# Kernel tuning notes

Measured on AMD Instinct MI355X. Metric: run time of the kernel, lower is better.

The kernel has to match this reference:

```python
import jax, jax.numpy as jnp
import numpy as np

EPS = 1e-6

def layernorm(x, alpha, bias):
    # torch.std default is unbiased (ddof=1)
    mean = x.mean(axis=-1, keepdims=True)
    std = jnp.std(x, axis=-1, keepdims=True, ddof=1)
    return alpha * (x - mean) / (std + EPS) + bias


def setup_inputs() -> dict:
    key = jax.random.key(0)
    B, L, d_model = 2, 1024, 1024
    d_state, d_conv, expand = 16, 4, 2
    d_inner = expand * d_model
    ks = jax.random.split(key, 8)
    std = 0.02
    x = jax.random.normal(ks[0], (B, L, d_model), dtype=jnp.float32)
    in_proj_w = jax.random.normal(ks[1], (2 * d_inner, d_model), dtype=jnp.float32) * std
    in_proj_b = jnp.zeros((2 * d_inner,), jnp.float32)
    conv_w = jax.random.normal(ks[2], (d_inner, 1, d_conv), dtype=jnp.float32) * std  # depthwise, groups=d_inner
    conv_b = jnp.zeros((d_inner,), jnp.float32)
    x_proj_w = jax.random.normal(ks[3], (2 * d_state, d_inner), dtype=jnp.float32) * std
    x_proj_b = jnp.zeros((2 * d_state,), jnp.float32)
    dt_proj_w = jax.random.normal(ks[4], (d_inner, d_inner), dtype=jnp.float32) * std
    dt_proj_b = jnp.zeros((d_inner,), jnp.float32)
    A_log = jnp.log(jnp.tile(jnp.arange(1, d_state + 1, dtype=jnp.float32), (d_inner, 1)))
    D = jnp.ones((d_inner,), jnp.float32)
    out_proj_w = jax.random.normal(ks[5], (d_model, d_inner), dtype=jnp.float32) * std
    out_proj_b = jnp.zeros((d_model,), jnp.float32)
    in_norm_alpha = jnp.ones((d_model,), jnp.float32)
    in_norm_bias = jnp.zeros((d_model,), jnp.float32)
    norm_alpha = jnp.ones((d_model,), jnp.float32)
    norm_bias = jnp.zeros((d_model,), jnp.float32)
    return {"x": x, "in_proj_w": in_proj_w, "in_proj_b": in_proj_b,
            "conv_w": conv_w, "conv_b": conv_b,
            "x_proj_w": x_proj_w, "x_proj_b": x_proj_b,
            "dt_proj_w": dt_proj_w, "dt_proj_b": dt_proj_b,
            "A_log": A_log, "D": D,
            "out_proj_w": out_proj_w, "out_proj_b": out_proj_b,
            "in_norm_alpha": in_norm_alpha, "in_norm_bias": in_norm_bias,
            "norm_alpha": norm_alpha, "norm_bias": norm_bias}


def reference(x, in_proj_w, in_proj_b, conv_w, conv_b, x_proj_w, x_proj_b,
              dt_proj_w, dt_proj_b, A_log, D, out_proj_w, out_proj_b,
              in_norm_alpha, in_norm_bias, norm_alpha, norm_bias):
    batch, L, d_model = x.shape
    d_inner = D.shape[0]
    d_state = A_log.shape[1]
    d_conv = conv_w.shape[-1]

    residual = x
    xn = layernorm(x, in_norm_alpha, in_norm_bias)
    xz = xn @ in_proj_w.T + in_proj_b                    # (B, L, 2*d_inner)
    x_in, z = jnp.split(xz, 2, axis=-1)

    # causal depthwise conv: torch pads both sides by d_conv-1 then slices [:L]
    # -> equivalent to left-pad only
    xc = jnp.swapaxes(x_in, 1, 2)                        # (B, d_inner, L)
    xc = jax.lax.conv_general_dilated(
        xc, conv_w, window_strides=(1,), padding=[(d_conv - 1, 0)],
        dimension_numbers=('NCH', 'OIH', 'NCH'),
        feature_group_count=d_inner) + conv_b[None, :, None]
    xc = jax.nn.silu(jnp.swapaxes(xc, 1, 2))             # (B, L, d_inner)

    Bmat, Cmat = jnp.split(xc @ x_proj_w.T + x_proj_b, 2, axis=-1)  # (B, L, d_state) each
    delta = jnp.clip(jax.nn.softplus(xc @ dt_proj_w.T + dt_proj_b), 1e-4, 10.0)
    A = -jnp.exp(A_log)                                  # (d_inner, d_state)
    flags = (jnp.arange(L) % 16) == 15                   # periodic renorm mask

    def step(h, inp):
        d_t, B_t, C_t, x_t, flag = inp                   # d_t,x_t: (B,d_inner); B_t,C_t: (B,d_state)
        dA = jnp.exp(jnp.clip(d_t[..., None] * A, -10.0, 0.0))      # (B,d_inner,d_state)
        dBx = d_t[..., None] * B_t[:, None, :] * x_t[..., None]
        h = dA * h + dBx
        hn = jnp.maximum(jnp.linalg.norm(h, axis=-1, keepdims=True), 1e-6)
        scale = jnp.where(hn > 10.0, 10.0 / hn, 1.0)
        h = jnp.where(flag, h * scale, h)
        y_t = jnp.sum(C_t[:, None, :] * h, axis=-1) + D * x_t
        return h, y_t

    h0 = jnp.zeros((batch, d_inner, d_state), dtype=x.dtype)
    xs = (jnp.swapaxes(delta, 0, 1), jnp.swapaxes(Bmat, 0, 1),
          jnp.swapaxes(Cmat, 0, 1), jnp.swapaxes(xc, 0, 1), flags)
    _, ys = jax.lax.scan(step, h0, xs)                   # ys: (L, B, d_inner)
    y = jnp.swapaxes(ys, 0, 1)

    y = y * jax.nn.silu(z)
    out = y @ out_proj_w.T + out_proj_b                  # dropout is identity in eval
    return layernorm(residual + out, norm_alpha, norm_bias)
```

## Files before the change

### kernel.cpp

```cpp
#include <hip/hip_runtime.h>
#include <math.h>

typedef unsigned short u16;
typedef unsigned int   u32;
typedef __bf16 bf16x8 __attribute__((ext_vector_type(8)));
typedef float  f32x4  __attribute__((ext_vector_type(4)));
typedef u16    u16x8  __attribute__((ext_vector_type(8)));

#define NB   2
#define LL   1024
#define DM   1024
#define DI   2048
#define MM   (NB*LL)
#define NXZ  (2*DI)
#define DSTATE 16
#define NSEG 64
#define NDT  2176
#define F32PAT 0x3F800000u

__device__ __forceinline__ float b2f(u16 u) {
  union { u32 i; float f; } v; v.i = ((u32)u) << 16; return v.f;
}
__device__ __forceinline__ u16 f2b(float f) {
  union { float f; u32 i; } v; v.f = f;
  u32 r = (v.i + 0x7FFFu + ((v.i >> 16) & 1u)) >> 16;
  return (u16)r;
}
__device__ __forceinline__ float ldx(const void* p, size_t i, bool isf32) {
  return isf32 ? ((const float*)p)[i] : b2f(((const u16*)p)[i]);
}

typedef __attribute__((address_space(1))) const void gas_t;
typedef __attribute__((address_space(3))) void las_t;
__device__ __forceinline__ void gload_lds16(const void* g, void* l) {
  __builtin_amdgcn_global_load_lds((gas_t*)g, (las_t*)l, 16, 0, 0);
}

__global__ __launch_bounds__(256) void ln1_kernel(
    const void* __restrict__ x, const void* __restrict__ alpha,
    const void* __restrict__ beta, u16* __restrict__ out,
    const u32* __restrict__ probe)
{
  const bool isf32 = (*probe == F32PAT);
  int row = blockIdx.x;
  int base = threadIdx.x * 4;
  size_t ix = (size_t)row * DM + base;
  float v0, v1, v2, v3;
  if (isf32) {
    float4 f = *(const float4*)((const float*)x + ix);
    v0 = f.x; v1 = f.y; v2 = f.z; v3 = f.w;
  } else {
    ushort4 u = *(const ushort4*)((const u16*)x + ix);
    v0 = b2f(u.x); v1 = b2f(u.y); v2 = b2f(u.z); v3 = b2f(u.w);
  }
  float s  = v0 + v1 + v2 + v3;
  float ss = v0*v0 + v1*v1 + v2*v2 + v3*v3;
#pragma unroll
  for (int off = 32; off > 0; off >>= 1) {
    s  += __shfl_down(s,  off);
    ss += __shfl_down(ss, off);
  }
  __shared__ float sb[4], ssb[4];
  int wv = threadIdx.x >> 6, ln = threadIdx.x & 63;
  if (ln == 0) { sb[wv] = s; ssb[wv] = ss; }
  __syncthreads();
  s  = sb[0]  + sb[1]  + sb[2]  + sb[3];
  ss = ssb[0] + ssb[1] + ssb[2] + ssb[3];
  float mean = s * (1.0f / DM);
  float var  = fmaxf((ss - (float)DM * mean * mean) * (1.0f / (DM - 1)), 0.0f);
  float inv  = 1.0f / (sqrtf(var) + 1e-6f);
  float a0 = ldx(alpha, base+0, isf32), a1 = ldx(alpha, base+1, isf32);
  float a2 = ldx(alpha, base+2, isf32), a3 = ldx(alpha, base+3, isf32);
  float b0 = ldx(beta,  base+0, isf32), b1 = ldx(beta,  base+1, isf32);
  float b2 = ldx(beta,  base+2, isf32), b3 = ldx(beta,  base+3, isf32);
  ushort4 o;
  o.x = f2b(a0 * (v0 - mean) * inv + b0);
  o.y = f2b(a1 * (v1 - mean) * inv + b1);
  o.z = f2b(a2 * (v2 - mean) * inv + b2);
  o.w = f2b(a3 * (v3 - mean) * inv + b3);
  *(ushort4*)(out + ix) = o;
}

__global__ __launch_bounds__(256) void ln2_kernel(
    const void* __restrict__ x, const float* __restrict__ outp,
    const void* __restrict__ alpha, const void* __restrict__ beta,
    void* __restrict__ out, const u32* __restrict__ probe)
{
  const bool isf32 = (*probe == F32PAT);
  int row = blockIdx.x;
  int base = threadIdx.x * 4;
  size_t ix = (size_t)row * DM + base;
  float v0, v1, v2, v3;
  if (isf32) {
    float4 f = *(const float4*)((const float*)x + ix);
    v0 = f.x; v1 = f.y; v2 = f.z; v3 = f.w;
  } else {
    ushort4 u = *(const ushort4*)((const u16*)x + ix);
    v0 = b2f(u.x); v1 = b2f(u.y); v2 = b2f(u.z); v3 = b2f(u.w);
  }
  float4 p = *(const float4*)(outp + ix);
  v0 += p.x; v1 += p.y; v2 += p.z; v3 += p.w;
  float s  = v0 + v1 + v2 + v3;
  float ss = v0*v0 + v1*v1 + v2*v2 + v3*v3;
#pragma unroll
  for (int off = 32; off > 0; off >>= 1) {
    s  += __shfl_down(s,  off);
    ss += __shfl_down(ss, off);
  }
  __shared__ float sb[4], ssb[4];
  int wv = threadIdx.x >> 6, ln = threadIdx.x & 63;
  if (ln == 0) { sb[wv] = s; ssb[wv] = ss; }
  __syncthreads();
  s  = sb[0]  + sb[1]  + sb[2]  + sb[3];
  ss = ssb[0] + ssb[1] + ssb[2] + ssb[3];
  float mean = s * (1.0f / DM);
  float var  = fmaxf((ss - (float)DM * mean * mean) * (1.0f / (DM - 1)), 0.0f);
  float inv  = 1.0f / (sqrtf(var) + 1e-6f);
  float a0 = ldx(alpha, base+0, isf32), a1 = ldx(alpha, base+1, isf32);
  float a2 = ldx(alpha, base+2, isf32), a3 = ldx(alpha, base+3, isf32);
  float b0 = ldx(beta,  base+0, isf32), b1 = ldx(beta,  base+1, isf32);
  float b2 = ldx(beta,  base+2, isf32), b3 = ldx(beta,  base+3, isf32);
  float r0 = a0 * (v0 - mean) * inv + b0;
  float r1 = a1 * (v1 - mean) * inv + b1;
  float r2 = a2 * (v2 - mean) * inv + b2;
  float r3 = a3 * (v3 - mean) * inv + b3;
  if (isf32) {
    float4 o; o.x = r0; o.y = r1; o.z = r2; o.w = r3;
    *(float4*)((float*)out + ix) = o;
  } else {
    ushort4 o; o.x = f2b(r0); o.y = f2b(r1); o.z = f2b(r2); o.w = f2b(r3);
    *(ushort4*)((u16*)out + ix) = o;
  }
}

__global__ __launch_bounds__(256) void ln2_sk_kernel(
    const void* __restrict__ x, const float* __restrict__ P,
    const void* __restrict__ op_bias,
    const void* __restrict__ alpha, const void* __restrict__ beta,
    void* __restrict__ out, const u32* __restrict__ probe)
{
  const bool isf32 = (*probe == F32PAT);
  int row = blockIdx.x;
  int base = threadIdx.x * 4;
  size_t ix = (size_t)row * DM + base;
  float v0, v1, v2, v3;
  if (isf32) {
    float4 f = *(const float4*)((const float*)x + ix);
    v0 = f.x; v1 = f.y; v2 = f.z; v3 = f.w;
  } else {
    ushort4 u = *(const ushort4*)((const u16*)x + ix);
    v0 = b2f(u.x); v1 = b2f(u.y); v2 = b2f(u.z); v3 = b2f(u.w);
  }
  v0 += ldx(op_bias, base+0, isf32);
  v1 += ldx(op_bias, base+1, isf32);
  v2 += ldx(op_bias, base+2, isf32);
  v3 += ldx(op_bias, base+3, isf32);
#pragma unroll
  for (int sk = 0; sk < 4; ++sk) {
    float4 p = *(const float4*)(P + ((size_t)sk * MM + row) * DM + base);
    v0 += p.x; v1 += p.y; v2 += p.z; v3 += p.w;
  }
  float s  = v0 + v1 + v2 + v3;
  float ss = v0*v0 + v1*v1 + v2*v2 + v3*v3;
#pragma unroll
  for (int off = 32; off > 0; off >>= 1) {
    s  += __shfl_down(s,  off);
    ss += __shfl_down(ss, off);
  }
  __shared__ float sb[4], ssb[4];
  int wv = threadIdx.x >> 6, ln = threadIdx.x & 63;
  if (ln == 0) { sb[wv] = s; ssb[wv] = ss; }
  __syncthreads();
  s  = sb[0]  + sb[1]  + sb[2]  + sb[3];
  ss = ssb[0] + ssb[1] + ssb[2] + ssb[3];
  float mean = s * (1.0f / DM);
  float var  = fmaxf((ss - (float)DM * mean * mean) * (1.0f / (DM - 1)), 0.0f);
  float inv  = 1.0f / (sqrtf(var) + 1e-6f);
  float a0 = ldx(alpha, base+0, isf32), a1 = ldx(alpha, base+1, isf32);
  float a2 = ldx(alpha, base+2, isf32), a3 = ldx(alpha, base+3, isf32);
  float b0 = ldx(beta,  base+0, isf32), b1 = ldx(beta,  base+1, isf32);
  float b2 = ldx(beta,  base+2, isf32), b3 = ldx(beta,  base+3, isf32);
  float r0 = a0 * (v0 - mean) * inv + b0;
  float r1 = a1 * (v1 - mean) * inv + b1;
  float r2 = a2 * (v2 - mean) * inv + b2;
  float r3 = a3 * (v3 - mean) * inv + b3;
  if (isf32) {
    float4 o; o.x = r0; o.y = r1; o.z = r2; o.w = r3;
    *(float4*)((float*)out + ix) = o;
  } else {
    ushort4 o; o.x = f2b(r0); o.y = f2b(r1); o.z = f2b(r2); o.w = f2b(r3);
    *(ushort4*)((u16*)out + ix) = o;
  }
}

#define CVT_A  4194304u
#define CVT_B  8388608u
#define CVT_C 10485760u
#define CVT_D 10551296u
#define CVT_E 10747904u

__global__ __launch_bounds__(256) void cvt_kernel(
    const void* __restrict__ s_in, const void* __restrict__ s_dt,
    const void* __restrict__ s_op, const void* __restrict__ s_xp,
    u16* __restrict__ inpw, u16* __restrict__ wdt, u16* __restrict__ opw,
    const u32* __restrict__ probe)
{
  const bool isf32 = (*probe == F32PAT);
  size_t i4 = ((size_t)blockIdx.x * 256 + threadIdx.x) * 4;
  if (i4 >= CVT_E) return;
  const void* src; u16* dst; size_t off;
  if      (i4 < CVT_A) { src = s_in; dst = inpw;        off = i4; }
  else if (i4 < CVT_B) { src = s_dt; dst = wdt;         off = i4 - CVT_A; }
  else if (i4 < CVT_C) { src = s_op; dst = opw;         off = i4 - CVT_B; }
  else if (i4 < CVT_D) { src = s_xp; dst = wdt + CVT_A; off = i4 - CVT_C; }
  else {
    ushort4 z = {0, 0, 0, 0};
    *(ushort4*)(wdt + 4259840u + (i4 - CVT_D)) = z;
    return;
  }
  ushort4 o;
  if (isf32) {
    float4 f = *(const float4*)((const float*)src + off);
    o.x = f2b(f.x); o.y = f2b(f.y); o.z = f2b(f.z); o.w = f2b(f.w);
  } else {
    o = *(const ushort4*)((const u16*)src + off);
  }
  *(ushort4*)(dst + off) = o;
}

#define EPI_NONE 0
#define EPI_SOFTPLUS 1

template<int EPI, int OUTBF>
__global__ __launch_bounds__(256) void gemm_fast(
    const u16* __restrict__ A, const u16* __restrict__ W,
    const void* __restrict__ bias, void* __restrict__ Cout,
    const u32* __restrict__ probe, int M, int N, int K)
{
  __shared__ __align__(16) u16 As[128 * 32];
  __shared__ __align__(16) u16 Ws[128 * 32];
  const bool isf32 = (*probe == F32PAT);
  const int tid  = threadIdx.x;
  const int wave = tid >> 6;
  const int lane = tid & 63;
  const int quad = lane >> 4;
  const int l16  = lane & 15;
  const int m0 = blockIdx.x * 128;
  const int n0 = blockIdx.y * 128;
  const int wm = (wave >> 1) * 64;
  const int wn = (wave & 1) * 64;

  f32x4 acc[4][4] = {};

  for (int k0 = 0; k0 < K; k0 += 32) {
    __syncthreads();
#pragma unroll
    for (int q = 0; q < 2; ++q) {
      int ci  = wave * 128 + q * 64 + lane;
      int row = ci >> 2;
      int kc  = (ci & 3) * 8;
      const u16* ga = A + (size_t)(m0 + row) * K + k0 + kc;
      const u16* gw = W + (size_t)(n0 + row) * K + k0 + kc;
      u16* la = As + (size_t)(wave * 128 + q * 64) * 8;
      u16* lw = Ws + (size_t)(wave * 128 + q * 64) * 8;
      gload_lds16(ga, la);
      gload_lds16(gw, lw);
    }
    __syncthreads();
    bf16x8 af[4], bfr[4];
#pragma unroll
    for (int i = 0; i < 4; ++i) {
      af[i]  = *(const bf16x8*)(As + (size_t)(wm + i * 16 + l16) * 32 + quad * 8);
      bfr[i] = *(const bf16x8*)(Ws + (size_t)(wn + i * 16 + l16) * 32 + quad * 8);
    }
#pragma unroll
    for (int i = 0; i < 4; ++i)
#pragma unroll
      for (int j = 0; j < 4; ++j)
        acc[i][j] = __builtin_amdgcn_mfma_f32_16x16x32_bf16(af[i], bfr[j], acc[i][j], 0, 0, 0);
  }

#pragma unroll
  for (int i = 0; i < 4; ++i) {
    int rbase = m0 + wm + i * 16 + quad * 4;
#pragma unroll
    for (int j = 0; j < 4; ++j) {
      int col = n0 + wn + j * 16 + l16;
      float bv = ldx(bias, col, isf32);
#pragma unroll
      for (int r = 0; r < 4; ++r) {
        float v = acc[i][j][r] + bv;
        if (EPI == EPI_SOFTPLUS) {
          v = (v > 20.0f) ? v : __logf(1.0f + __expf(v));
          v = fminf(fmaxf(v, 1e-4f), 10.0f);
        }
        size_t oi = (size_t)(rbase + r) * N + col;
        if (OUTBF) ((u16*)Cout)[oi] = f2b(v);
        else       ((float*)Cout)[oi] = v;
      }
    }
  }
}

__global__ __launch_bounds__(256) void gemm_sk(
    const u16* __restrict__ A, const u16* __restrict__ W,
    float* __restrict__ P, int M, int N, int Kfull, int Kslice)
{
  __shared__ __align__(16) u16 As[128 * 32];
  __shared__ __align__(16) u16 Ws[128 * 32];
  const int tid  = threadIdx.x;
  const int wave = tid >> 6;
  const int lane = tid & 63;
  const int quad = lane >> 4;
  const int l16  = lane & 15;
  const int m0 = blockIdx.x * 128;
  const int n0 = blockIdx.y * 128;
  const int sk = blockIdx.z;
  const int kbeg = sk * Kslice;
  const int kend = kbeg + Kslice;
  const int wm = (wave >> 1) * 64;
  const int wn = (wave & 1) * 64;

  f32x4 acc[4][4] = {};

  for (int k0 = kbeg; k0 < kend; k0 += 32) {
    __syncthreads();
#pragma unroll
    for (int q = 0; q < 2; ++q) {
      int ci  = wave * 128 + q * 64 + lane;
      int row = ci >> 2;
      int kc  = (ci & 3) * 8;
      const u16* ga = A + (size_t)(m0 + row) * Kfull + k0 + kc;
      const u16* gw = W + (size_t)(n0 + row) * Kfull + k0 + kc;
      u16* la = As + (size_t)(wave * 128 + q * 64) * 8;
      u16* lw = Ws + (size_t)(wave * 128 + q * 64) * 8;
      gload_lds16(ga, la);
      gload_lds16(gw, lw);
    }
    __syncthreads();
    bf16x8 af[4], bfr[4];
#pragma unroll
    for (int i = 0; i < 4; ++i) {
      af[i]  = *(const bf16x8*)(As + (size_t)(wm + i * 16 + l16) * 32 + quad * 8);
      bfr[i] = *(const bf16x8*)(Ws + (size_t)(wn + i * 16 + l16) * 32 + quad * 8);
    }
#pragma unroll
    for (int i = 0; i < 4; ++i)
#pragma unroll
      for (int j = 0; j < 4; ++j)
        acc[i][j] = __builtin_amdgcn_mfma_f32_16x16x32_bf16(af[i], bfr[j], acc[i][j], 0, 0, 0);
  }

  float* Pb = P + (size_t)sk * M * N;
#pragma unroll
  for (int i = 0; i < 4; ++i) {
    int rbase = m0 + wm + i * 16 + quad * 4;
#pragma unroll
    for (int j = 0; j < 4; ++j) {
      int col = n0 + wn + j * 16 + l16;
#pragma unroll
      for (int r = 0; r < 4; ++r)
        Pb[(size_t)(rbase + r) * N + col] = acc[i][j][r];
    }
  }
}

__global__ __launch_bounds__(256) void reduce_combo(
    const float* __restrict__ P, const void* __restrict__ bias_dt,
    const void* __restrict__ bias_xp, float* __restrict__ delta,
    float* __restrict__ bc, const u32* __restrict__ probe)
{
  const bool isf32 = (*probe == F32PAT);
  const int m = blockIdx.x;
  const float* p0 = P + (size_t)m * NDT;
  const float* p1 = P + (size_t)(MM + m) * NDT;
  for (int n = threadIdx.x; n < DI + 32; n += 256) {
    float v = p0[n] + p1[n];
    if (n < DI) {
      v += ldx(bias_dt, n, isf32);
      v = (v > 20.0f) ? v : __logf(1.0f + __expf(v));
      v = fminf(fmaxf(v, 1e-4f), 10.0f);
      delta[(size_t)m * DI + n] = v;
    } else {
      bc[(size_t)m * 32 + (n - DI)] = v + ldx(bias_xp, n - DI, isf32);
    }
  }
}

template<int EPI, int OUTBF>
__global__ __launch_bounds__(256) void gemm_r2(
    const u16* __restrict__ A, const void* __restrict__ W,
    const void* __restrict__ bias, void* __restrict__ Cout,
    const u32* __restrict__ probe, int M, int N, int K)
{
  __shared__ __align__(16) u16 As[128 * 32];
  __shared__ __align__(16) u16 Ws[128 * 32];
  const bool isf32 = (*probe == F32PAT);
  const int tid  = threadIdx.x;
  const int wave = tid >> 6;
  const int lane = tid & 63;
  const int quad = lane >> 4;
  const int l16  = lane & 15;
  const int m0 = blockIdx.x * 128;
  const int n0 = blockIdx.y * 128;
  const int wm = (wave >> 1) * 64;
  const int wn = (wave & 1) * 64;

  f32x4 acc[4][4] = {};

  for (int k0 = 0; k0 < K; k0 += 32) {
    u16x8 va[2], vw[2];
#pragma unroll
    for (int q = 0; q < 2; ++q) {
      int ci  = wave * 128 + q * 64 + lane;
      int row = ci >> 2;
      int kc  = (ci & 3) * 8;
      va[q] = *(const u16x8*)(A + (size_t)(m0 + row) * K + k0 + kc);
      size_t wi = (size_t)(n0 + row) * K + k0 + kc;
      if (isf32) {
        const float* Wf = (const float*)W;
        float4 f0 = *(const float4*)(Wf + wi);
        float4 f1 = *(const float4*)(Wf + wi + 4);
        u16x8 t;
        t[0] = f2b(f0.x); t[1] = f2b(f0.y); t[2] = f2b(f0.z); t[3] = f2b(f0.w);
        t[4] = f2b(f1.x); t[5] = f2b(f1.y); t[6] = f2b(f1.z); t[7] = f2b(f1.w);
        vw[q] = t;
      } else {
        vw[q] = *(const u16x8*)((const u16*)W + wi);
      }
    }
    __syncthreads();
#pragma unroll
    for (int q = 0; q < 2; ++q) {
      int ci = wave * 128 + q * 64 + lane;
      *(u16x8*)(As + (size_t)ci * 8) = va[q];
      *(u16x8*)(Ws + (size_t)ci * 8) = vw[q];
    }
    __syncthreads();
    bf16x8 af[4], bfr[4];
#pragma unroll
    for (int i = 0; i < 4; ++i) {
      af[i]  = *(const bf16x8*)(As + (size_t)(wm + i * 16 + l16) * 32 + quad * 8);
      bfr[i] = *(const bf16x8*)(Ws + (size_t)(wn + i * 16 + l16) * 32 + quad * 8);
    }
#pragma unroll
    for (int i = 0; i < 4; ++i)
#pragma unroll
      for (int j = 0; j < 4; ++j)
        acc[i][j] = __builtin_amdgcn_mfma_f32_16x16x32_bf16(af[i], bfr[j], acc[i][j], 0, 0, 0);
  }

#pragma unroll
  for (int i = 0; i < 4; ++i) {
    int rbase = m0 + wm + i * 16 + quad * 4;
#pragma unroll
    for (int j = 0; j < 4; ++j) {
      int col = n0 + wn + j * 16 + l16;
      float bv = ldx(bias, col, isf32);
#pragma unroll
      for (int r = 0; r < 4; ++r) {
        float v = acc[i][j][r] + bv;
        if (EPI == EPI_SOFTPLUS) {
          v = (v > 20.0f) ? v : __logf(1.0f + __expf(v));
          v = fminf(fmaxf(v, 1e-4f), 10.0f);
        }
        size_t oi = (size_t)(rbase + r) * N + col;
        if (OUTBF) ((u16*)Cout)[oi] = f2b(v);
        else       ((float*)Cout)[oi] = v;
      }
    }
  }
}

__global__ __launch_bounds__(256) void conv_silu_kernel(
    const u16* __restrict__ xz, const void* __restrict__ cw,
    const void* __restrict__ cb, u16* __restrict__ xc_bf,
    const u32* __restrict__ probe)
{
  const bool isf32 = (*probe == F32PAT);
  int g = blockIdx.x * 256 + threadIdx.x;
  int c = g & (DI - 1);
  int m = g >> 11;
  int l = m & (LL - 1);
  float w0 = ldx(cw, c*4+0, isf32), w1 = ldx(cw, c*4+1, isf32);
  float w2 = ldx(cw, c*4+2, isf32), w3 = ldx(cw, c*4+3, isf32);
  const u16* col = xz + (size_t)m * NXZ + c;
  float acc = ldx(cb, c, isf32);
  acc += w3 * b2f(col[0]);
  if (l >= 1) acc += w2 * b2f(*(col - NXZ));
  if (l >= 2) acc += w1 * b2f(*(col - 2*NXZ));
  if (l >= 3) acc += w0 * b2f(*(col - 3*NXZ));
  float sil = acc / (1.0f + __expf(-acc));
  xc_bf[g] = f2b(sil);
}

__global__ __launch_bounds__(256) void proj_bc_r2(
    const u16* __restrict__ xc, const void* __restrict__ W,
    const void* __restrict__ bias, float* __restrict__ bc,
    const u32* __restrict__ probe)
{
  const bool isf32 = (*probe == F32PAT);
  int m = blockIdx.x;
  int n = threadIdx.x >> 3;
  int part = threadIdx.x & 7;
  const u16* xr = xc + (size_t)m * DI + part * 256;
  size_t wbase = (size_t)n * DI + part * 256;
  float acc = 0.0f;
  if (isf32) {
    const float* wr = (const float*)W + wbase;
#pragma unroll 8
    for (int i = 0; i < 256; i += 4) {
      ushort4 xv = *(const ushort4*)(xr + i);
      float4  wv = *(const float4*)(wr + i);
      acc += b2f(xv.x)*wv.x + b2f(xv.y)*wv.y + b2f(xv.z)*wv.z + b2f(xv.w)*wv.w;
    }
  } else {
    const u16* wr = (const u16*)W + wbase;
#pragma unroll 8
    for (int i = 0; i < 256; i += 4) {
      ushort4 xv = *(const ushort4*)(xr + i);
      ushort4 wv = *(const ushort4*)(wr + i);
      acc += b2f(xv.x)*b2f(wv.x) + b2f(xv.y)*b2f(wv.y)
           + b2f(xv.z)*b2f(wv.z) + b2f(xv.w)*b2f(wv.w);
    }
  }
  __shared__ float ps[256];
  ps[threadIdx.x] = acc;
  __syncthreads();
  if (threadIdx.x < 32) {
    float s = 0.0f;
#pragma unroll
    for (int p = 0; p < 8; ++p) s += ps[threadIdx.x * 8 + p];
    bc[(size_t)m * 32 + threadIdx.x] = s + ldx(bias, threadIdx.x, isf32);
  }
}

__global__ __launch_bounds__(256, 4) void scan_p1(
    const float* __restrict__ delta, const float* __restrict__ bc,
    const u16* __restrict__ xc, const void* __restrict__ A_log,
    float2* __restrict__ PQ, const u32* __restrict__ probe)
{
  const bool isf32 = (*probe == F32PAT);
  const int c = blockIdx.x * 256 + threadIdx.x;
  const int g = blockIdx.y;
  const int b = blockIdx.z;
  const int row0 = b * LL + g * 16;
  __shared__ float sBC[512];
  if (threadIdx.x < 128)
    *(float4*)&sBC[threadIdx.x * 4] =
        *(const float4*)(bc + (size_t)row0 * 32 + threadIdx.x * 4);
  float Av2[16];
#pragma unroll
  for (int s = 0; s < 16; ++s)
    Av2[s] = -__expf(ldx(A_log, (size_t)c * DSTATE + s, isf32)) * 1.44269504f;
  float p[16], q[16];
#pragma unroll
  for (int s = 0; s < 16; ++s) { p[s] = 1.0f; q[s] = 0.0f; }
  __syncthreads();
  const float CLIP2 = -14.4269504f;
#pragma unroll 4
  for (int j = 0; j < 16; ++j) {
    int row = row0 + j;
    float d  = delta[(size_t)row * DI + c];
    float x  = b2f(xc[(size_t)row * DI + c]);
    float dx = d * x;
    float4 B4[4];
    B4[0] = *(const float4*)&sBC[j * 32 + 0];
    B4[1] = *(const float4*)&sBC[j * 32 + 4];
    B4[2] = *(const float4*)&sBC[j * 32 + 8];
    B4[3] = *(const float4*)&sBC[j * 32 + 12];
    const float* Bv = (const float*)B4;
#pragma unroll
    for (int s = 0; s < 16; ++s) {
      float a = __builtin_amdgcn_exp2f(fmaxf(d * Av2[s], CLIP2));
      q[s] = a * q[s] + dx * Bv[s];
      p[s] *= a;
    }
  }
  float2* out = PQ + ((size_t)(b * NSEG + g) * DI + c) * DSTATE;
#pragma unroll
  for (int s = 0; s < 16; ++s) out[s] = make_float2(p[s], q[s]);
}

__global__ __launch_bounds__(256) void scan_p2(
    const float2* __restrict__ PQ, float* __restrict__ Hin,
    float* __restrict__ Scale)
{
  const int s = threadIdx.x & 15;
  const int c = blockIdx.x * 16 + (threadIdx.x >> 4);
  const int b = blockIdx.y;
  const size_t stride = (size_t)DI * DSTATE;
  const size_t base = ((size_t)b * NSEG * DI + c) * DSTATE + s;
  float h = 0.0f;
  float2 pq = PQ[base];
  for (int g = 0; g < NSEG; ++g) {
    float2 cur = pq;
    if (g < NSEG - 1) pq = PQ[base + (size_t)(g + 1) * stride];
    Hin[base + (size_t)g * stride] = h;
    h = cur.x * h + cur.y;
    float n2 = h * h;
    n2 += __shfl_xor(n2, 1);
    n2 += __shfl_xor(n2, 2);
    n2 += __shfl_xor(n2, 4);
    n2 += __shfl_xor(n2, 8);
    float hn = fmaxf(sqrtf(n2), 1e-6f);
    float sc = hn > 10.0f ? 10.0f / hn : 1.0f;
    if (s == 0) Scale[((size_t)b * NSEG + g) * DI + c] = sc;
    h *= sc;
  }
}

__global__ __launch_bounds__(256, 4) void scan_p3(
    const float* __restrict__ delta, const float* __restrict__ bc,
    const u16* __restrict__ xc, const u16* __restrict__ xz,
    const void* __restrict__ A_log, const void* __restrict__ Dp,
    const float* __restrict__ Hin, const float* __restrict__ Scale,
    u16* __restrict__ y_bf, const u32* __restrict__ probe)
{
  const bool isf32 = (*probe == F32PAT);
  const int c = blockIdx.x * 256 + threadIdx.x;
  const int g = blockIdx.y;
  const int b = blockIdx.z;
  const int row0 = b * LL + g * 16;
  __shared__ float sBC[512];
  if (threadIdx.x < 128)
    *(float4*)&sBC[threadIdx.x * 4] =
        *(const float4*)(bc + (size_t)row0 * 32 + threadIdx.x * 4);
  float Av2[16];
#pragma unroll
  for (int s = 0; s < 16; ++s)
    Av2[s] = -__expf(ldx(A_log, (size_t)c * DSTATE + s, isf32)) * 1.44269504f;
  float h[16];
  const float* hp = Hin + ((size_t)(b * NSEG + g) * DI + c) * DSTATE;
#pragma unroll
  for (int s4 = 0; s4 < 4; ++s4)
    *(float4*)&h[s4 * 4] = *(const float4*)(hp + s4 * 4);
  const float sc15 = Scale[((size_t)b * NSEG + g) * DI + c];
  const float Dc = ldx(Dp, c, isf32);
  __syncthreads();
  const float CLIP2 = -14.4269504f;
#pragma unroll 4
  for (int j = 0; j < 16; ++j) {
    int row = row0 + j;
    float d  = delta[(size_t)row * DI + c];
    float x  = b2f(xc[(size_t)row * DI + c]);
    float z  = b2f(xz[(size_t)row * NXZ + DI + c]);
    float dx = d * x;
    float4 BC[8];
    BC[0] = *(const float4*)&sBC[j * 32 + 0];
    BC[1] = *(const float4*)&sBC[j * 32 + 4];
    BC[2] = *(const float4*)&sBC[j * 32 + 8];
    BC[3] = *(const float4*)&sBC[j * 32 + 12];
    BC[4] = *(const float4*)&sBC[j * 32 + 16];
    BC[5] = *(const float4*)&sBC[j * 32 + 20];
    BC[6] = *(const float4*)&sBC[j * 32 + 24];
    BC[7] = *(const float4*)&sBC[j * 32 + 28];
    const float* Bv = (const float*)BC;
    const float* Cv = Bv + 16;
#pragma unroll
    for (int s = 0; s < 16; ++s) {
      float a = __builtin_amdgcn_exp2f(fmaxf(d * Av2[s], CLIP2));
      h[s] = a * h[s] + dx * Bv[s];
    }
    if (j == 15) {
#pragma unroll
      for (int s = 0; s < 16; ++s) h[s] *= sc15;
    }
    float ys = 0.0f;
#pragma unroll
    for (int s = 0; s < 16; ++s) ys += Cv[s] * h[s];
    float yo = (ys + Dc * x) * (z / (1.0f + __expf(-z)));
    y_bf[(size_t)row * DI + c] = f2b(yo);
  }
}

__global__ __launch_bounds__(256) void scan_mono(
    const float* __restrict__ delta, const float* __restrict__ bc,
    const u16* __restrict__ xc, const u16* __restrict__ xz,
    const void* __restrict__ A_log, const void* __restrict__ Dp,
    u16* __restrict__ y_bf, const u32* __restrict__ probe)
{
  const bool isf32 = (*probe == F32PAT);
  const int s = threadIdx.x & 15;
  const int c = blockIdx.x * 16 + (threadIdx.x >> 4);
  const int b = blockIdx.y;
  const float Av2 = -__expf(ldx(A_log, (size_t)c * DSTATE + s, isf32)) * 1.44269504f;
  const float Dc  = ldx(Dp, c, isf32);
  const float CLIP2 = -14.4269504f;
  float h = 0.0f;
  for (int t0 = 0; t0 < LL; t0 += 16) {
    float dl[16], xl[16], zl[16], Bv[16], Cv[16];
#pragma unroll
    for (int j = 0; j < 16; ++j) {
      int row = b * LL + t0 + j;
      dl[j] = delta[(size_t)row * DI + c];
      xl[j] = b2f(xc[(size_t)row * DI + c]);
      zl[j] = b2f(xz[(size_t)row * NXZ + DI + c]);
      Bv[j] = bc[(size_t)row * 32 + s];
      Cv[j] = bc[(size_t)row * 32 + 16 + s];
    }
#pragma unroll
    for (int j = 0; j < 16; ++j) {
      float d = dl[j], x = xl[j];
      float dA = __builtin_amdgcn_exp2f(fmaxf(d * Av2, CLIP2));
      h = dA * h + (d * x) * Bv[j];
      if (j == 15) {
        float n2 = h * h;
        n2 += __shfl_xor(n2, 1); n2 += __shfl_xor(n2, 2);
        n2 += __shfl_xor(n2, 4); n2 += __shfl_xor(n2, 8);
        float hn = fmaxf(sqrtf(n2), 1e-6f);
        float sc = hn > 10.0f ? 10.0f / hn : 1.0f;
        h *= sc;
      }
      float ys = Cv[j] * h;
      ys += __shfl_xor(ys, 1); ys += __shfl_xor(ys, 2);
      ys += __shfl_xor(ys, 4); ys += __shfl_xor(ys, 8);
      float z = zl[j];
      float yo = (ys + Dc * x) * (z / (1.0f + __expf(-z)));
      if (s == 0) {
        int row = b * LL + t0 + j;
        y_bf[(size_t)row * DI + c] = f2b(yo);
      }
    }
  }
}

extern "C" void kernel_launch(void* const* d_in, const int* in_sizes, int n_in,
                              void* d_out, int out_size, void* d_ws, size_t ws_size,
                              hipStream_t stream) {
  const void* x          = d_in[0];
  const void* in_proj_w  = d_in[1];
  const void* in_proj_b  = d_in[2];
  const void* conv_w     = d_in[3];
  const void* conv_b     = d_in[4];
  const void* x_proj_w   = d_in[5];
  const void* x_proj_b   = d_in[6];
  const void* dt_proj_w  = d_in[7];
  const void* dt_proj_b  = d_in[8];
  const void* A_log      = d_in[9];
  const void* Dp         = d_in[10];
  const void* out_proj_w = d_in[11];
  const void* out_proj_b = d_in[12];
  const void* in_norm_a  = d_in[13];
  const void* in_norm_b  = d_in[14];
  const void* norm_a     = d_in[15];
  const void* norm_b     = d_in[16];
  const u32*  probe      = (const u32*)d_in[13];

  const size_t MiB = 1048576;
  const size_t NEED_NEW = 106299392;

  if (ws_size >= NEED_NEW) {
    char* w = (char*)d_ws;
    u16*   xz_bf = (u16*)w;    w += 16 * MiB;
    u16*   xc_bf = (u16*)w;    w += 8 * MiB;
    float* delta = (float*)w;  w += 16 * MiB;
    float* bc    = (float*)w;  w += 256 * 1024;
    float* Scale = (float*)w;  w += 1 * MiB;
    u16*   opw   = (u16*)w;    w += 4 * MiB;
    u16*   y_bf  = (u16*)w;    w += 8 * MiB;
    char* S = w;
    u16*    wdt    = (u16*)(S);
    u16*    inpw   = (u16*)(S + 8*MiB + 512*1024);
    u16*    xn_bf  = (u16*)(S + 16*MiB + 512*1024);
    float*  deltaP = (float*)(S + 8*MiB + 512*1024);
    float2* PQ     = (float2*)(S);
    float*  Hin    = (float*)(S + 32*MiB);
    float*  outP   = (float*)(S);

    cvt_kernel<<<10496, 256, 0, stream>>>(in_proj_w, dt_proj_w, out_proj_w, x_proj_w,
                                          inpw, wdt, opw, probe);
    ln1_kernel<<<MM, 256, 0, stream>>>(x, in_norm_a, in_norm_b, xn_bf, probe);
    gemm_fast<EPI_NONE, 1><<<dim3(MM/128, NXZ/128), 256, 0, stream>>>(
        xn_bf, inpw, in_proj_b, xz_bf, probe, MM, NXZ, DM);
    conv_silu_kernel<<<(MM * DI) / 256, 256, 0, stream>>>(xz_bf, conv_w, conv_b, xc_bf, probe);
    gemm_sk<<<dim3(MM/128, NDT/128, 2), 256, 0, stream>>>(
        xc_bf, wdt, deltaP, MM, NDT, DI, DI/2);
    reduce_combo<<<MM, 256, 0, stream>>>(deltaP, dt_proj_b, x_proj_b, delta, bc, probe);
    scan_p1<<<dim3(DI/256, NSEG, NB), 256, 0, stream>>>(delta, bc, xc_bf, A_log, PQ, probe);
    scan_p2<<<dim3(DI/16, NB), 256, 0, stream>>>(PQ, Hin, Scale);
    scan_p3<<<dim3(DI/256, NSEG, NB), 256, 0, stream>>>(
        delta, bc, xc_bf, xz_bf, A_log, Dp, Hin, Scale, y_bf, probe);
    gemm_sk<<<dim3(MM/128, DM/128, 4), 256, 0, stream>>>(
        y_bf, opw, outP, MM, DM, DI, DI/4);
    ln2_sk_kernel<<<MM, 256, 0, stream>>>(x, outP, out_proj_b, norm_a, norm_b, d_out, probe);
  } else {
    char* w = (char*)d_ws;
    u16*   xn_bf = (u16*)w;   w += (size_t)MM * DM * 2;
    u16*   xz_bf = (u16*)w;   w += (size_t)MM * NXZ * 2;
    u16*   xc_bf = (u16*)w;   w += (size_t)MM * DI * 2;
    float* delta = (float*)w; w += (size_t)MM * DI * 4;
    float* bc    = (float*)w; w += (size_t)MM * 32 * 4;
    u16*   y_bf  = (u16*)w;   w += (size_t)MM * DI * 2;
    float* outp  = (float*)w; w += (size_t)MM * DM * 4;

    ln1_kernel<<<MM, 256, 0, stream>>>(x, in_norm_a, in_norm_b, xn_bf, probe);
    gemm_r2<EPI_NONE, 1><<<dim3(MM/128, NXZ/128), 256, 0, stream>>>(
        xn_bf, in_proj_w, in_proj_b, xz_bf, probe, MM, NXZ, DM);
    conv_silu_kernel<<<(MM * DI) / 256, 256, 0, stream>>>(xz_bf, conv_w, conv_b, xc_bf, probe);
    gemm_r2<EPI_SOFTPLUS, 0><<<dim3(MM/128, DI/128), 256, 0, stream>>>(
        xc_bf, dt_proj_w, dt_proj_b, delta, probe, MM, DI, DI);
    proj_bc_r2<<<MM, 256, 0, stream>>>(xc_bf, x_proj_w, x_proj_b, bc, probe);
    scan_mono<<<dim3(DI/16, NB), 256, 0, stream>>>(delta, bc, xc_bf, xz_bf, A_log, Dp, y_bf, probe);
    gemm_r2<EPI_NONE, 0><<<dim3(MM/128, DM/128), 256, 0, stream>>>(
        y_bf, out_proj_w, out_proj_b, outp, probe, MM, DM, DI);
    ln2_kernel<<<MM, 256, 0, stream>>>(x, outp, norm_a, norm_b, d_out, probe);
  }
}
```

Before: 346.6 us.

## Use K=64 swizzled LDS tiles and fuse dt/x projection epilogue without split-K

The GEMM kernels now stage 64-wide K tiles into LDS with an XOR swizzle, which halves the number of barrier pairs per K and is meant to reduce LDS bank conflicts. The dt/x projection split-K GEMM plus its separate reduce kernel is replaced by a single non-split GEMM that applies bias, softplus and clamping in its epilogue and writes delta and bc directly. This removes the partial-sum round trip through memory and one launch, but lowers parallelism for that GEMM (half as many blocks) and doubles LDS per block, which may reduce occupancy.

```diff
diff --git a/kernel.cpp b/kernel.cpp
--- a/kernel.cpp
+++ b/kernel.cpp
@@ -228,6 +228,25 @@
   *(ushort4*)(dst + off) = o;
 }
 
+__device__ __forceinline__ void stage64(const u16* __restrict__ G, int rowK,
+                                        int k0, u16* __restrict__ lds,
+                                        int wave, int lane, int m0) {
+#pragma unroll
+  for (int q = 0; q < 4; ++q) {
+    int ci = (wave * 4 + q) * 64 + lane;
+    int r  = ci >> 3;
+    int s  = ci & 7;
+    int ch = s ^ (r & 7);
+    const u16* ga = G + (size_t)(m0 + r) * rowK + k0 + ch * 8;
+    gload_lds16(ga, lds + (size_t)ci * 8);
+  }
+}
+__device__ __forceinline__ bf16x8 frag64(const u16* __restrict__ lds,
+                                         int r, int ch) {
+  int s = ch ^ (r & 7);
+  return *(const bf16x8*)(lds + (size_t)r * 64 + s * 8);
+}
+
 #define EPI_NONE 0
 #define EPI_SOFTPLUS 1
 
@@ -237,8 +256,8 @@
     const void* __restrict__ bias, void* __restrict__ Cout,
     const u32* __restrict__ probe, int M, int N, int K)
 {
-  __shared__ __align__(16) u16 As[128 * 32];
-  __shared__ __align__(16) u16 Ws[128 * 32];
+  __shared__ __align__(16) u16 As[128 * 64];
+  __shared__ __align__(16) u16 Ws[128 * 64];
   const bool isf32 = (*probe == F32PAT);
   const int tid  = threadIdx.x;
   const int wave = tid >> 6;
@@ -252,32 +271,25 @@
 
   f32x4 acc[4][4] = {};
 
-  for (int k0 = 0; k0 < K; k0 += 32) {
+  for (int k0 = 0; k0 < K; k0 += 64) {
     __syncthreads();
-#pragma unroll
-    for (int q = 0; q < 2; ++q) {
-      int ci  = wave * 128 + q * 64 + lane;
-      int row = ci >> 2;
-      int kc  = (ci & 3) * 8;
-      const u16* ga = A + (size_t)(m0 + row) * K + k0 + kc;
-      const u16* gw = W + (size_t)(n0 + row) * K + k0 + kc;
-      u16* la = As + (size_t)(wave * 128 + q * 64) * 8;
-      u16* lw = Ws + (size_t)(wave * 128 + q * 64) * 8;
-      gload_lds16(ga, la);
-      gload_lds16(gw, lw);
-    }
+    stage64(A, K, k0, As, wave, lane, m0);
+    stage64(W, K, k0, Ws, wave, lane, n0);
     __syncthreads();
-    bf16x8 af[4], bfr[4];
-#pragma unroll
-    for (int i = 0; i < 4; ++i) {
-      af[i]  = *(const bf16x8*)(As + (size_t)(wm + i * 16 + l16) * 32 + quad * 8);
-      bfr[i] = *(const bf16x8*)(Ws + (size_t)(wn + i * 16 + l16) * 32 + quad * 8);
-    }
-#pragma unroll
-    for (int i = 0; i < 4; ++i)
-#pragma unroll
-      for (int j = 0; j < 4; ++j)
-        acc[i][j] = __builtin_amdgcn_mfma_f32_16x16x32_bf16(af[i], bfr[j], acc[i][j], 0, 0, 0);
+#pragma unroll
+    for (int kk = 0; kk < 2; ++kk) {
+      bf16x8 af[4], bfr[4];
+#pragma unroll
+      for (int i = 0; i < 4; ++i) {
+        af[i]  = frag64(As, wm + i * 16 + l16, kk * 4 + quad);
+        bfr[i] = frag64(Ws, wn + i * 16 + l16, kk * 4 + quad);
+      }
+#pragma unroll
+      for (int i = 0; i < 4; ++i)
+#pragma unroll
+        for (int j = 0; j < 4; ++j)
+          acc[i][j] = __builtin_amdgcn_mfma_f32_16x16x32_bf16(af[i], bfr[j], acc[i][j], 0, 0, 0);
+    }
   }
 
 #pragma unroll
@@ -302,12 +314,79 @@
   }
 }
 
+__global__ __launch_bounds__(256) void gemm_combo(
+    const u16* __restrict__ A, const u16* __restrict__ W,
+    const void* __restrict__ bias_dt, const void* __restrict__ bias_xp,
+    float* __restrict__ delta, float* __restrict__ bc,
+    const u32* __restrict__ probe, int K)
+{
+  __shared__ __align__(16) u16 As[128 * 64];
+  __shared__ __align__(16) u16 Ws[128 * 64];
+  const bool isf32 = (*probe == F32PAT);
+  const int tid  = threadIdx.x;
+  const int wave = tid >> 6;
+  const int lane = tid & 63;
+  const int quad = lane >> 4;
+  const int l16  = lane & 15;
+  const int m0 = blockIdx.x * 128;
+  const int n0 = blockIdx.y * 128;
+  const int wm = (wave >> 1) * 64;
+  const int wn = (wave & 1) * 64;
+
+  f32x4 acc[4][4] = {};
+
+  for (int k0 = 0; k0 < K; k0 += 64) {
+    __syncthreads();
+    stage64(A, K, k0, As, wave, lane, m0);
+    stage64(W, K, k0, Ws, wave, lane, n0);
+    __syncthreads();
+#pragma unroll
+    for (int kk = 0; kk < 2; ++kk) {
+      bf16x8 af[4], bfr[4];
+#pragma unroll
+      for (int i = 0; i < 4; ++i) {
+        af[i]  = frag64(As, wm + i * 16 + l16, kk * 4 + quad);
+        bfr[i] = frag64(Ws, wn + i * 16 + l16, kk * 4 + quad);
+      }
+#pragma unroll
+      for (int i = 0; i < 4; ++i)
+#pragma unroll
+        for (int j = 0; j < 4; ++j)
+          acc[i][j] = __builtin_amdgcn_mfma_f32_16x16x32_bf16(af[i], bfr[j], acc[i][j], 0, 0, 0);
+    }
+  }
+
+#pragma unroll
+  for (int i = 0; i < 4; ++i) {
+    int rbase = m0 + wm + i * 16 + quad * 4;
+#pragma unroll
+    for (int j = 0; j < 4; ++j) {
+      int col = n0 + wn + j * 16 + l16;
+      if (col < DI) {
+        float bv = ldx(bias_dt, col, isf32);
+#pragma unroll
+        for (int r = 0; r < 4; ++r) {
+          float v = acc[i][j][r] + bv;
+          v = (v > 20.0f) ? v : __logf(1.0f + __expf(v));
+          v = fminf(fmaxf(v, 1e-4f), 10.0f);
+          delta[(size_t)(rbase + r) * DI + col] = v;
+        }
+      } else if (col < DI + 32) {
+        float bv = ldx(bias_xp, col - DI, isf32);
+#pragma unroll
+        for (int r = 0; r < 4; ++r)
+          bc[(size_t)(rbase + r) * 32 + (col - DI)] = acc[i][j][r] + bv;
+      }
+    }
+  }
+}
+
 __global__ __launch_bounds__(256) void gemm_sk(
     const u16* __restrict__ A, const u16* __restrict__ W,
     float* __restrict__ P, int M, int N, int Kfull, int Kslice)
 {
-  __shared__ __align__(16) u16 As[128 * 32];
-  __shared__ __align__(16) u16 Ws[128 * 32];
+  __shared__ __align__(16) u16 As[128 * 64];
+  __shared__ __align__(16) u16 Ws[128 * 64];
   const int tid  = threadIdx.x;
   const int wave = tid >> 6;
   const int lane = tid & 63;
@@ -323,32 +402,25 @@
 
   f32x4 acc[4][4] = {};
 
-  for (int k0 = kbeg; k0 < kend; k0 += 32) {
+  for (int k0 = kbeg; k0 < kend; k0 += 64) {
     __syncthreads();
-#pragma unroll
-    for (int q = 0; q < 2; ++q) {
-      int ci  = wave * 128 + q * 64 + lane;
-      int row = ci >> 2;
-      int kc  = (ci & 3) * 8;
-      const u16* ga = A + (size_t)(m0 + row) * Kfull + k0 + kc;
-      const u16* gw = W + (size_t)(n0 + row) * Kfull + k0 + kc;
-      u16* la = As + (size_t)(wave * 128 + q * 64) * 8;
-      u16* lw = Ws + (size_t)(wave * 128 + q * 64) * 8;
-      gload_lds16(ga, la);
-      gload_lds16(gw, lw);
-    }
+    stage64(A, Kfull, k0, As, wave, lane, m0);
+    stage64(W, Kfull, k0, Ws, wave, lane, n0);
     __syncthreads();
-    bf16x8 af[4], bfr[4];
-#pragma unroll
-    for (int i = 0; i < 4; ++i) {
-      af[i]  = *(const bf16x8*)(As + (size_t)(wm + i * 16 + l16) * 32 + quad * 8);
-      bfr[i] = *(const bf16x8*)(Ws + (size_t)(wn + i * 16 + l16) * 32 + quad * 8);
-    }
-#pragma unroll
-    for (int i = 0; i < 4; ++i)
-#pragma unroll
-      for (int j = 0; j < 4; ++j)
-        acc[i][j] = __builtin_amdgcn_mfma_f32_16x16x32_bf16(af[i], bfr[j], acc[i][j], 0, 0, 0);
+#pragma unroll
+    for (int kk = 0; kk < 2; ++kk) {
+      bf16x8 af[4], bfr[4];
+#pragma unroll
+      for (int i = 0; i < 4; ++i) {
+        af[i]  = frag64(As, wm + i * 16 + l16, kk * 4 + quad);
+        bfr[i] = frag64(Ws, wn + i * 16 + l16, kk * 4 + quad);
+      }
+#pragma unroll
+      for (int i = 0; i < 4; ++i)
+#pragma unroll
+        for (int j = 0; j < 4; ++j)
+          acc[i][j] = __builtin_amdgcn_mfma_f32_16x16x32_bf16(af[i], bfr[j], acc[i][j], 0, 0, 0);
+    }
   }
 
   float* Pb = P + (size_t)sk * M * N;
@@ -361,28 +433,6 @@
 #pragma unroll
       for (int r = 0; r < 4; ++r)
         Pb[(size_t)(rbase + r) * N + col] = acc[i][j][r];
-    }
-  }
-}
-
-__global__ __launch_bounds__(256) void reduce_combo(
-    const float* __restrict__ P, const void* __restrict__ bias_dt,
-    const void* __restrict__ bias_xp, float* __restrict__ delta,
-    float* __restrict__ bc, const u32* __restrict__ probe)
-{
-  const bool isf32 = (*probe == F32PAT);
-  const int m = blockIdx.x;
-  const float* p0 = P + (size_t)m * NDT;
-  const float* p1 = P + (size_t)(MM + m) * NDT;
-  for (int n = threadIdx.x; n < DI + 32; n += 256) {
-    float v = p0[n] + p1[n];
-    if (n < DI) {
-      v += ldx(bias_dt, n, isf32);
-      v = (v > 20.0f) ? v : __logf(1.0f + __expf(v));
-      v = fminf(fmaxf(v, 1e-4f), 10.0f);
-      delta[(size_t)m * DI + n] = v;
-    } else {
-      bc[(size_t)m * 32 + (n - DI)] = v + ldx(bias_xp, n - DI, isf32);
     }
   }
 }
@@ -763,7 +813,6 @@
     u16*    wdt    = (u16*)(S);
     u16*    inpw   = (u16*)(S + 8*MiB + 512*1024);
     u16*    xn_bf  = (u16*)(S + 16*MiB + 512*1024);
-    float*  deltaP = (float*)(S + 8*MiB + 512*1024);
     float2* PQ     = (float2*)(S);
     float*  Hin    = (float*)(S + 32*MiB);
     float*  outP   = (float*)(S);
@@ -774,9 +823,8 @@
     gemm_fast<EPI_NONE, 1><<<dim3(MM/128, NXZ/128), 256, 0, stream>>>(
         xn_bf, inpw, in_proj_b, xz_bf, probe, MM, NXZ, DM);
     conv_silu_kernel<<<(MM * DI) / 256, 256, 0, stream>>>(xz_bf, conv_w, conv_b, xc_bf, probe);
-    gemm_sk<<<dim3(MM/128, NDT/128, 2), 256, 0, stream>>>(
-        xc_bf, wdt, deltaP, MM, NDT, DI, DI/2);
-    reduce_combo<<<MM, 256, 0, stream>>>(deltaP, dt_proj_b, x_proj_b, delta, bc, probe);
+    gemm_combo<<<dim3(MM/128, NDT/128), 256, 0, stream>>>(
+        xc_bf, wdt, dt_proj_b, x_proj_b, delta, bc, probe, DI);
     scan_p1<<<dim3(DI/256, NSEG, NB), 256, 0, stream>>>(delta, bc, xc_bf, A_log, PQ, probe);
     scan_p2<<<dim3(DI/16, NB), 256, 0, stream>>>(PQ, Hin, Scale);
     scan_p3<<<dim3(DI/256, NSEG, NB), 256, 0, stream>>>(
```

New measurement: 328.9 us. 1.05x faster.
